# Performance work log

Measured on AMD Instinct MI355X. Metric: run time of the kernel, lower is better.

The kernel has to match this reference:

```python
import jax, jax.numpy as jnp
import numpy as np

E = 16_000_000          # number of edges (nnz of sparse adj)
N_NODES = 500_000       # node id range for COO indices
KEEP_RATE = 0.5


def setup_inputs() -> dict:
    key = jax.random.key(0)
    k1, k2, k3 = jax.random.split(key, 3)
    vals = jax.random.uniform(k1, (E,), dtype=jnp.float32)
    idxs = jax.random.randint(k2, (2, E), 0, N_NODES, dtype=jnp.int64 if jax.config.read('jax_enable_x64') else jnp.int32)
    rand_u = jax.random.uniform(k3, (E,), dtype=jnp.float32)
    keep_rate = jnp.float32(KEEP_RATE)
    return {"vals": vals, "idxs": idxs, "rand_u": rand_u, "keep_rate": keep_rate}


def reference(vals, idxs, rand_u, keep_rate):
    # torch: mask = (rand(E) + keepRate).floor().bool(); newVals = vals[mask]/keepRate
    # jit-friendly equivalent: keep full index set, zero out dropped edge values.
    mask = jnp.floor(rand_u + keep_rate).astype(jnp.bool_)
    new_vals = jnp.where(mask, vals / keep_rate, jnp.float32(0.0))
    # (new_vals, idxs) together represent sparse_coo_tensor(newIdxs, newVals, shape)
    return new_vals, idxs
```

## Files before the change

### kernel.cpp

```cpp
#include <hip/hip_runtime.h>

typedef float  float4_t __attribute__((ext_vector_type(4)));
typedef int    int4_t   __attribute__((ext_vector_type(4)));

__global__ void SpAdjDropEdge_48541720379660_kernel(
    const float* __restrict__ vals,
    const int*   __restrict__ idxs,
    const float* __restrict__ rand_u,
    const float* __restrict__ keep_rate_p,
    float*       __restrict__ out,
    int nv4, int ni4)
{
    const float kr = keep_rate_p[0];
    const int total  = nv4 + ni4;
    const int stride = gridDim.x * blockDim.x;

    for (int i = blockIdx.x * blockDim.x + threadIdx.x; i < total; i += stride) {
        if (i < nv4) {
            float4_t v = reinterpret_cast<const float4_t*>(vals)[i];
            float4_t r = reinterpret_cast<const float4_t*>(rand_u)[i];
            float4_t o;
#pragma unroll
            for (int j = 0; j < 4; ++j) {
                bool keep = (floorf(r[j] + kr) != 0.0f);
                o[j] = keep ? (v[j] / kr) : 0.0f;
            }
            reinterpret_cast<float4_t*>(out)[i] = o;
        } else {
            const int k = i - nv4;
            int4_t id = reinterpret_cast<const int4_t*>(idxs)[k];
            float4_t o;
#pragma unroll
            for (int j = 0; j < 4; ++j) {
                o[j] = (float)id[j];
            }
            reinterpret_cast<float4_t*>(out + (size_t)nv4 * 4)[k] = o;
        }
    }
}

extern "C" void kernel_launch(void* const* d_in, const int* in_sizes, int n_in,
                              void* d_out, int out_size, void* d_ws, size_t ws_size,
                              hipStream_t stream)
{
    const float* vals   = (const float*)d_in[0];
    const int*   idxs   = (const int*)  d_in[1];
    const float* rand_u = (const float*)d_in[2];
    const float* kr     = (const float*)d_in[3];
    float*       out    = (float*)d_out;

    const int E  = in_sizes[0];
    const int NI = in_sizes[1];
    const int nv4 = E  / 4;
    const int ni4 = NI / 4;

    const int block = 256;
    const int grid  = 4096;

    SpAdjDropEdge_48541720379660_kernel<<<grid, block, 0, stream>>>(
        vals, idxs, rand_u, kr, out, nv4, ni4);
}
```

Baseline: 90.53 us.

## Split grid into value and index blocks with unrolled batched loads

Replaces the fixed-size grid-stride loop with a grid sized to cover all work exactly. Blocks are partitioned into a value-processing set and an index-conversion set, which removes per-iteration branching. Each thread issues four independent vector loads before computing, which raises memory-level parallelism. The cost is a much larger grid, with tens of thousands of blocks instead of 4096.

```diff
diff --git a/kernel.cpp b/kernel.cpp
--- a/kernel.cpp
+++ b/kernel.cpp
@@ -2,6 +2,8 @@
 
 typedef float  float4_t __attribute__((ext_vector_type(4)));
 typedef int    int4_t   __attribute__((ext_vector_type(4)));
+
+#define UNROLL 4
 
 __global__ void SpAdjDropEdge_48541720379660_kernel(
     const float* __restrict__ vals,
@@ -9,32 +11,64 @@
     const float* __restrict__ rand_u,
     const float* __restrict__ keep_rate_p,
     float*       __restrict__ out,
-    int nv4, int ni4)
+    int nv4, int ni4, int blocksV)
 {
-    const float kr = keep_rate_p[0];
-    const int total  = nv4 + ni4;
-    const int stride = gridDim.x * blockDim.x;
+    if ((int)blockIdx.x < blocksV) {
+        const int t      = blockIdx.x * blockDim.x + threadIdx.x;
+        const int stride = blocksV * blockDim.x;
+        const float kr   = keep_rate_p[0];
 
-    for (int i = blockIdx.x * blockDim.x + threadIdx.x; i < total; i += stride) {
-        if (i < nv4) {
-            float4_t v = reinterpret_cast<const float4_t*>(vals)[i];
-            float4_t r = reinterpret_cast<const float4_t*>(rand_u)[i];
-            float4_t o;
+        int  idx_[UNROLL];
+        bool ok_[UNROLL];
+        float4_t v_[UNROLL], r_[UNROLL];
 #pragma unroll
-            for (int j = 0; j < 4; ++j) {
-                bool keep = (floorf(r[j] + kr) != 0.0f);
-                o[j] = keep ? (v[j] / kr) : 0.0f;
+        for (int k = 0; k < UNROLL; ++k) {
+            idx_[k] = t + k * stride;
+            ok_[k]  = idx_[k] < nv4;
+        }
+#pragma unroll
+        for (int k = 0; k < UNROLL; ++k)
+            if (ok_[k]) v_[k] = reinterpret_cast<const float4_t*>(vals)[idx_[k]];
+#pragma unroll
+        for (int k = 0; k < UNROLL; ++k)
+            if (ok_[k]) r_[k] = reinterpret_cast<const float4_t*>(rand_u)[idx_[k]];
+#pragma unroll
+        for (int k = 0; k < UNROLL; ++k) {
+            if (ok_[k]) {
+                float4_t o;
+#pragma unroll
+                for (int j = 0; j < 4; ++j) {
+                    bool keep = (floorf(r_[k][j] + kr) != 0.0f);
+                    o[j] = keep ? (v_[k][j] / kr) : 0.0f;
+                }
+                reinterpret_cast<float4_t*>(out)[idx_[k]] = o;
             }
-            reinterpret_cast<float4_t*>(out)[i] = o;
-        } else {
-            const int k = i - nv4;
-            int4_t id = reinterpret_cast<const int4_t*>(idxs)[k];
-            float4_t o;
+        }
+    } else {
+        const int t      = (blockIdx.x - blocksV) * blockDim.x + threadIdx.x;
+        const int stride = (gridDim.x - blocksV) * blockDim.x;
+        float* outi = out + (size_t)nv4 * 4;
+
+        int  idx_[UNROLL];
+        bool ok_[UNROLL];
+        int4_t a_[UNROLL];
 #pragma unroll
-            for (int j = 0; j < 4; ++j) {
-                o[j] = (float)id[j];
+        for (int k = 0; k < UNROLL; ++k) {
+            idx_[k] = t + k * stride;
+            ok_[k]  = idx_[k] < ni4;
+        }
+#pragma unroll
+        for (int k = 0; k < UNROLL; ++k)
+            if (ok_[k]) a_[k] = reinterpret_cast<const int4_t*>(idxs)[idx_[k]];
+#pragma unroll
+        for (int k = 0; k < UNROLL; ++k) {
+            if (ok_[k]) {
+                float4_t o;
+#pragma unroll
+                for (int j = 0; j < 4; ++j)
+                    o[j] = (float)a_[k][j];
+                reinterpret_cast<float4_t*>(outi)[idx_[k]] = o;
             }
-            reinterpret_cast<float4_t*>(out + (size_t)nv4 * 4)[k] = o;
         }
     }
 }
@@ -54,9 +88,12 @@
     const int nv4 = E  / 4;
     const int ni4 = NI / 4;
 
-    const int block = 256;
-    const int grid  = 4096;
+    const int block   = 256;
+    const int perBlk  = block * UNROLL;
+    const int blocksV = (nv4 + perBlk - 1) / perBlk;
+    const int blocksI = (ni4 + perBlk - 1) / perBlk;
+    const int grid    = blocksV + blocksI;
 
     SpAdjDropEdge_48541720379660_kernel<<<grid, block, 0, stream>>>(
-        vals, idxs, rand_u, kr, out, nv4, ni4);
+        vals, idxs, rand_u, kr, out, nv4, ni4, blocksV);
 }
```

Result: faster. 87.36 us (-3.5%).
